# Performance work log

Measured on AMD Instinct MI355X. Metric: run time of the kernel, lower is better.

The kernel has to match this reference:

```python
import jax, jax.numpy as jnp
import numpy as np

B, D, H = 128, 256, 512  # batch, input_size, hidden_size; 2 hidden layers
ORDER = 'A'
EPS = 1e-12


def _masks():
    # Standard MADE sequential degrees: inputs 1..D (reversed for order 'B'),
    # hidden degrees cycle over 1..D-1. Hidden mask: >=, output mask: > (strict).
    din = np.arange(1, D + 1) if ORDER == 'A' else np.arange(D, 0, -1)
    dh = (np.arange(H) % (D - 1)) + 1
    m0 = (dh[:, None] >= din[None, :]).astype(np.float32)  # [H, D]
    m1 = (dh[:, None] >= dh[None, :]).astype(np.float32)   # [H, H]
    mo = (din[:, None] > dh[None, :]).astype(np.float32)   # [D, H]
    return jnp.asarray(m0), jnp.asarray(m1), jnp.asarray(mo)


def _made(y, W0, b0, W1, b1, Wo, bo, masks):
    m0, m1, mo = masks
    h = jax.nn.elu(y @ (W0 * m0).T + b0)   # [B, H]
    h = jax.nn.elu(h @ (W1 * m1).T + b1)   # [B, H]
    return h @ (Wo * mo).T + bo            # [B, D]


def setup_inputs() -> dict:
    key = jax.random.key(0)
    ks = jax.random.split(key, 13)
    s_in, s_h = 1.0 / np.sqrt(D), 1.0 / np.sqrt(H)

    def p(k, shape, s):
        return (jax.random.normal(k, shape, jnp.float32) * s).astype(jnp.float32)

    return {
        'x': jax.random.normal(ks[0], (B, D), jnp.float32),
        'mu_W0': p(ks[1], (H, D), s_in), 'mu_b0': jnp.zeros((H,), jnp.float32),
        'mu_W1': p(ks[2], (H, H), s_h),  'mu_b1': jnp.zeros((H,), jnp.float32),
        'mu_Wo': p(ks[3], (D, H), s_h),  'mu_bo': jnp.zeros((D,), jnp.float32),
        'lv_W0': p(ks[4], (H, D), s_in), 'lv_b0': jnp.zeros((H,), jnp.float32),
        'lv_W1': p(ks[5], (H, H), s_h),  'lv_b1': jnp.zeros((H,), jnp.float32),
        'lv_Wo': p(ks[6], (D, H), s_h),  'lv_bo': jnp.zeros((D,), jnp.float32),
    }


def reference(x, mu_W0, mu_b0, mu_W1, mu_b1, mu_Wo, mu_bo,
              lv_W0, lv_b0, lv_W1, lv_b1, lv_Wo, lv_bo):
    masks = _masks()
    idx = jnp.arange(D) if ORDER == 'A' else jnp.arange(D - 1, -1, -1)

    def step(carry, i):
        y, _ = carry
        mu = _made(y, mu_W0, mu_b0, mu_W1, mu_b1, mu_Wo, mu_bo, masks)
        logstd = 0.5 * _made(y, lv_W0, lv_b0, lv_W1, lv_b1, lv_Wo, lv_bo, masks)
        new_col = (x[:, i] - mu[:, i]) / (jnp.exp(logstd[:, i]) + EPS)
        y = y.at[:, i].set(new_col)
        return (y, logstd), None

    init = (jnp.zeros_like(x), jnp.zeros_like(x))
    (y, logstd), _ = jax.lax.scan(step, init, idx)
    return y, logstd.sum(axis=1)
```

## Files before the change

kernel.cpp:

```cpp
#include <hip/hip_runtime.h>

#define DD 256
#define HH 512
#define BB 128
#define TS 4096

#define WAITVM(N) asm volatile("s_waitcnt vmcnt(" #N ")" ::: "memory")
#define SYNC() do { __builtin_amdgcn_s_barrier(); __builtin_amdgcn_sched_barrier(0); } while (0)

__device__ __forceinline__ float elu_f(float x) {
    return x > 0.f ? x : (__expf(x) - 1.f);
}
__device__ __forceinline__ float rlf(float v, int l) {
    return __uint_as_float(__builtin_amdgcn_readlane(__float_as_uint(v), (unsigned)l));
}
__device__ __forceinline__ float f4c(const float4& v, int r) {
    return r == 0 ? v.x : r == 1 ? v.y : r == 2 ? v.z : v.w;
}

__device__ __forceinline__ int pmap(int h) {
    if (h == 510) return 255;
    if (h == 511) return 511;
    return (h < 255) ? (4 * (h & 63) + (h >> 6))
                     : (256 + 4 * ((h - 255) & 63) + ((h - 255) >> 6));
}
__device__ __forceinline__ int p4map(int j) {
    return 4 * (j & 63) + (j >> 6);
}
__device__ __forceinline__ int w1base(int hp) {
    return (hp <= 254) ? hp * TS
         : (hp <= 509) ? (hp - 255) * TS + 1024
         : 255 * TS + ((hp == 510) ? 0 : 1024);
}
__device__ __forceinline__ int wobase(int hp) {
    return (hp <= 254) ? hp * TS + 3072
         : (hp <= 509) ? (hp - 255) * TS + 3584
         : 255 * TS + ((hp == 510) ? 2048 : 2560);
}

__global__ __launch_bounds__(256) void prep(
    const float* __restrict__ w0m_, const float* __restrict__ w0l_,
    const float* __restrict__ w1m_, const float* __restrict__ w1l_,
    const float* __restrict__ wom_, const float* __restrict__ wol_,
    float* __restrict__ tape)
{
    __shared__ float tm[32][33], tl[32][33];
    const int tx = threadIdx.x & 31, ty = threadIdx.x >> 5;
    const unsigned b = blockIdx.x;

    if (b < 256) {
        const int h0 = (int)(b >> 4) << 5, hp0 = (int)(b & 15) << 5;
        #pragma unroll
        for (int j = 0; j < 4; ++j) {
            int r = ty + 8 * j;
            tm[r][tx] = w1m_[(h0 + r) * HH + hp0 + tx];
            tl[r][tx] = w1l_[(h0 + r) * HH + hp0 + tx];
        }
        __syncthreads();
        #pragma unroll
        for (int j = 0; j < 4; ++j) {
            int hp = hp0 + ty + 8 * j;
            int h  = h0 + tx;
            int dh_h = (h <= 254) ? h + 1 : (h <= 509 ? h - 254 : h - 509);
            int dh_p = (hp <= 254) ? hp + 1 : (hp <= 509 ? hp - 254 : hp - 509);
            float mask = (dh_h >= dh_p) ? 1.f : 0.f;
            int base = w1base(hp), p = pmap(h);
            tape[base + p]       = mask * tm[tx][ty + 8 * j];
            tape[base + 512 + p] = mask * tl[tx][ty + 8 * j];
        }
    } else if (b < 384) {
        const int b2 = (int)b - 256;
        const int h0 = (b2 >> 3) << 5, i0 = (b2 & 7) << 5;
        #pragma unroll
        for (int j = 0; j < 4; ++j) {
            int r = ty + 8 * j;
            tm[r][tx] = w0m_[(h0 + r) * DD + i0 + tx];
            tl[r][tx] = w0l_[(h0 + r) * DD + i0 + tx];
        }
        __syncthreads();
        #pragma unroll
        for (int j = 0; j < 4; ++j) {
            int i = i0 + ty + 8 * j;
            int h = h0 + tx;
            int p = pmap(h);
            tape[i * TS + 2048 + p] = tm[tx][ty + 8 * j];
            tape[i * TS + 2560 + p] = tl[tx][ty + 8 * j];
        }
    } else {
        const int b3 = (int)b - 384;
        const int j0 = (b3 >> 4) << 5, hp0 = (b3 & 15) << 5;
        #pragma unroll
        for (int j = 0; j < 4; ++j) {
            int r = ty + 8 * j;
            tm[r][tx] = wom_[(j0 + r) * HH + hp0 + tx];
            tl[r][tx] = wol_[(j0 + r) * HH + hp0 + tx];
        }
        __syncthreads();
        #pragma unroll
        for (int j = 0; j < 4; ++j) {
            int hp = hp0 + ty + 8 * j;
            int jj = j0 + tx;
            int base = wobase(hp), p = p4map(jj);
            tape[base + p]       = tm[tx][ty + 8 * j];
            tape[base + 256 + p] = tl[tx][ty + 8 * j];
        }
    }
}

struct WSet { float4 w[16]; };

__device__ __forceinline__ void stage16(const float* g, float* l, int lane) {
    #pragma unroll
    for (int k = 0; k < 16; ++k) {
        __builtin_amdgcn_global_load_lds(
            (const __attribute__((address_space(1))) void*)(g + 256 * k + 4 * lane),
            (__attribute__((address_space(3))) void*)(l + 256 * k),
            16, 0, 0);
    }
}

__device__ __forceinline__ void rd_set(WSet& S, const float* b, int lane) {
    const float4* p = (const float4*)b;
    #pragma unroll
    for (int k = 0; k < 16; ++k) S.w[k] = p[64 * k + lane];
}

template<int Q, int EX>
__device__ __forceinline__ void stepC(
    int t, int lane, const WSet& S,
    float (&a0m)[8], float (&a0l)[8], float (&a1m)[8], float (&a1l)[8],
    float (&Rm)[4], float (&Rl)[4], float (&yv)[4],
    const float (&xv)[4], const float (&bmv)[4], const float (&blv)[4],
    float& ls_sum,
    const float4& exmA, const float4& exmB, const float4& exlA, const float4& exlB,
    const float4& exwm, const float4& exwl)
{
    float mu = rlf(Rm[Q], t) + rlf(bmv[Q], t);
    float ls = 0.5f * (rlf(Rl[Q], t) + rlf(blv[Q], t));
    ls_sum += ls;
    float v = __fdividef(rlf(xv[Q], t) - mu, __expf(ls) + 1e-12f);
    yv[Q] = (lane == t) ? v : yv[Q];

    #pragma unroll
    for (int r = Q; r < 4; ++r) {
        a0m[r]     += v * f4c(S.w[8], r);
        a0m[4 + r] += v * f4c(S.w[9], r);
        a0l[r]     += v * f4c(S.w[10], r);
        a0l[4 + r] += v * f4c(S.w[11], r);
    }

    float p0m = elu_f(rlf(a0m[Q], t)),     p0l = elu_f(rlf(a0l[Q], t));
    float p1m = elu_f(rlf(a0m[4 + Q], t)), p1l = elu_f(rlf(a0l[4 + Q], t));
    float p2m = 0.f, p2l = 0.f;
    if (EX) {
        p2m = elu_f(rlf(a0m[EX == 1 ? 3 : 7], 63));
        p2l = elu_f(rlf(a0l[EX == 1 ? 3 : 7], 63));
    }

    #pragma unroll
    for (int r = Q; r < 4; ++r) {
        a1m[r]     += f4c(S.w[0], r) * p0m + f4c(S.w[4], r) * p1m;
        a1m[4 + r] += f4c(S.w[1], r) * p0m + f4c(S.w[5], r) * p1m;
        a1l[r]     += f4c(S.w[2], r) * p0l + f4c(S.w[6], r) * p1l;
        a1l[4 + r] += f4c(S.w[3], r) * p0l + f4c(S.w[7], r) * p1l;
    }
    if (EX) {
        #pragma unroll
        for (int r = 0; r < 4; ++r) {
            a1m[r]     += f4c(exmA, r) * p2m;
            a1m[4 + r] += f4c(exmB, r) * p2m;
            a1l[r]     += f4c(exlA, r) * p2l;
            a1l[4 + r] += f4c(exlB, r) * p2l;
        }
    }

    float q0m = elu_f(rlf(a1m[Q], t)),     q0l = elu_f(rlf(a1l[Q], t));
    float q1m = elu_f(rlf(a1m[4 + Q], t)), q1l = elu_f(rlf(a1l[4 + Q], t));
    float q2m = 0.f, q2l = 0.f;
    if (EX) {
        q2m = elu_f(rlf(a1m[EX == 1 ? 3 : 7], 63));
        q2l = elu_f(rlf(a1l[EX == 1 ? 3 : 7], 63));
    }

    #pragma unroll
    for (int r = Q; r < 4; ++r) {
        Rm[r] += f4c(S.w[12], r) * q0m + f4c(S.w[14], r) * q1m;
        Rl[r] += f4c(S.w[13], r) * q0l + f4c(S.w[15], r) * q1l;
    }
    if (EX) {
        #pragma unroll
        for (int r = 0; r < 4; ++r) {
            Rm[r] += f4c(exwm, r) * q2m;
            Rl[r] += f4c(exwl, r) * q2l;
        }
    }
}

__global__ __launch_bounds__(128, 1) void made_main(
    const float* __restrict__ x,
    const float* __restrict__ mu_b0, const float* __restrict__ mu_b1,
    const float* __restrict__ mu_bo,
    const float* __restrict__ lv_b0, const float* __restrict__ lv_b1,
    const float* __restrict__ lv_bo,
    const float* __restrict__ tape,
    float* __restrict__ out)
{
    __shared__ __align__(16) float buf[4][TS];
    const int row = blockIdx.x;

    if (threadIdx.x >= 64) {
        const int lane = threadIdx.x - 64;
        #pragma unroll
        for (int g = 0; g < 3; ++g)
            stage16(tape + (size_t)g * TS, &buf[g][0], lane);
        #pragma unroll 1
        for (int t = 0; t < 255; ++t) {
            if (t < 253) { WAITVM(16); } else { WAITVM(0); }
            __builtin_amdgcn_s_barrier();
            __builtin_amdgcn_sched_barrier(0);
            int g = t + 3;
            if (g < 255)
                stage16(tape + (size_t)g * TS, &buf[g & 3][0], lane);
        }
        return;
    }

    const int lane = threadIdx.x;

    float a0m[8], a0l[8], a1m[8], a1l[8], Rm[4], Rl[4], yv[4];
    float xv[4], bmv[4], blv[4];
    #pragma unroll
    for (int r = 0; r < 4; ++r) {
        a0m[r]     = mu_b0[lane + 64 * r];
        a0m[4 + r] = mu_b0[255 + lane + 64 * r];
        a0l[r]     = lv_b0[lane + 64 * r];
        a0l[4 + r] = lv_b0[255 + lane + 64 * r];
        a1m[r]     = mu_b1[lane + 64 * r];
        a1m[4 + r] = mu_b1[255 + lane + 64 * r];
        a1l[r]     = lv_b1[lane + 64 * r];
        a1l[4 + r] = lv_b1[255 + lane + 64 * r];
        Rm[r] = 0.f; Rl[r] = 0.f; yv[r] = 0.f;
        xv[r]  = x[row * DD + 64 * r + lane];
        bmv[r] = mu_bo[64 * r + lane];
        blv[r] = lv_bo[64 * r + lane];
    }
    if (lane == 63) {
        a0m[3] = mu_b0[510]; a0m[7] = mu_b0[511];
        a0l[3] = lv_b0[510]; a0l[7] = lv_b0[511];
        a1m[3] = mu_b1[510]; a1m[7] = mu_b1[511];
        a1l[3] = lv_b1[510]; a1l[7] = lv_b1[511];
    }

    const float4* a4 = (const float4*)(tape + 255 * TS);
    float4 e510mA = a4[lane],       e510mB = a4[64 + lane];
    float4 e510lA = a4[128 + lane], e510lB = a4[192 + lane];
    float4 e511mA = a4[256 + lane], e511mB = a4[320 + lane];
    float4 e511lA = a4[384 + lane], e511lB = a4[448 + lane];
    float4 wo510m = a4[512 + lane], wo510l = a4[576 + lane];
    float4 wo511m = a4[640 + lane], wo511l = a4[704 + lane];

    const float4 d4 = make_float4(0.f, 0.f, 0.f, 0.f);

    float ls_sum = 0.f;
    WSet A, B;

    SYNC();
    rd_set(A, &buf[0][0], lane);
    rd_set(B, &buf[1][0], lane);
    stepC<0, 1>(0, lane, A, a0m, a0l, a1m, a1l, Rm, Rl, yv, xv, bmv, blv,
                ls_sum, e510mA, e510mB, e510lA, e510lB, wo510m, wo510l);

    SYNC();
    rd_set(A, &buf[2][0], lane);
    stepC<0, 2>(1, lane, B, a0m, a0l, a1m, a1l, Rm, Rl, yv, xv, bmv, blv,
                ls_sum, e511mA, e511mB, e511lA, e511lB, wo511m, wo511l);

#define PAIR_BODY(Q, t, tl)                                                   \
    {                                                                         \
        SYNC();                                                               \
        rd_set(B, &buf[((t) + 1) & 3][0], lane);                              \
        stepC<Q, 0>((tl), lane, A, a0m, a0l, a1m, a1l, Rm, Rl, yv,            \
                    xv, bmv, blv, ls_sum, d4, d4, d4, d4, d4, d4);            \
        SYNC();                                                               \
        rd_set(A, &buf[((t) + 2) & 3][0], lane);                              \
        stepC<Q, 0>((tl) + 1, lane, B, a0m, a0l, a1m, a1l, Rm, Rl, yv,        \
                    xv, bmv, blv, ls_sum, d4, d4, d4, d4, d4, d4);            \
    }

    #pragma unroll 1
    for (int t = 2; t < 64; t += 2)    PAIR_BODY(0, t, t)
    #pragma unroll 1
    for (int t = 64; t < 128; t += 2)  PAIR_BODY(1, t, t - 64)
    #pragma unroll 1
    for (int t = 128; t < 192; t += 2) PAIR_BODY(2, t, t - 128)
    #pragma unroll 1
    for (int t = 192; t < 254; t += 2) PAIR_BODY(3, t, t - 192)
#undef PAIR_BODY

    SYNC();
    stepC<3, 0>(62, lane, A, a0m, a0l, a1m, a1l, Rm, Rl, yv, xv, bmv, blv,
                ls_sum, d4, d4, d4, d4, d4, d4);

    {
        float mu = rlf(Rm[3], 63) + rlf(bmv[3], 63);
        float ls = 0.5f * (rlf(Rl[3], 63) + rlf(blv[3], 63));
        ls_sum += ls;
        float v = __fdividef(rlf(xv[3], 63) - mu, __expf(ls) + 1e-12f);
        yv[3] = (lane == 63) ? v : yv[3];
    }

    #pragma unroll
    for (int r = 0; r < 4; ++r) out[row * DD + 64 * r + lane] = yv[r];
    if (lane == 0) out[BB * DD + row] = ls_sum;
}

extern "C" void kernel_launch(void* const* d_in, const int* in_sizes, int n_in,
                              void* d_out, int out_size, void* d_ws, size_t ws_size,
                              hipStream_t stream) {
    const float* x     = (const float*)d_in[0];
    const float* mu_W0 = (const float*)d_in[1];
    const float* mu_b0 = (const float*)d_in[2];
    const float* mu_W1 = (const float*)d_in[3];
    const float* mu_b1 = (const float*)d_in[4];
    const float* mu_Wo = (const float*)d_in[5];
    const float* mu_bo = (const float*)d_in[6];
    const float* lv_W0 = (const float*)d_in[7];
    const float* lv_b0 = (const float*)d_in[8];
    const float* lv_W1 = (const float*)d_in[9];
    const float* lv_b1 = (const float*)d_in[10];
    const float* lv_Wo = (const float*)d_in[11];
    const float* lv_bo = (const float*)d_in[12];

    float* tape = (float*)d_ws;

    prep<<<512, 256, 0, stream>>>(mu_W0, lv_W0, mu_W1, lv_W1, mu_Wo, lv_Wo, tape);
    made_main<<<BB, 128, 0, stream>>>(x, mu_b0, mu_b1, mu_bo,
                                      lv_b0, lv_b1, lv_bo, tape, (float*)d_out);
}
```

Measured before the change: 183.1 us.

## Stage tape in pairs to halve producer-consumer barriers per step

The producer wave now loads two tape slices per barrier into a double-buffered pair of slots. The consumer reads both slices and runs two steps between barriers instead of one. This halves the number of workgroup barriers in the serial 255-step loop. In exchange, prefetch depth drops from three slices in flight to a wait-all per pair, so load latency is less hidden, and register pressure rises because two weight sets are live at once.

Measured after the change: 185.9 us. No clear change (+1.5%).

```diff
diff --git a/kernel.cpp b/kernel.cpp
--- a/kernel.cpp
+++ b/kernel.cpp
@@ -210,17 +210,17 @@
 
     if (threadIdx.x >= 64) {
         const int lane = threadIdx.x - 64;
-        #pragma unroll
-        for (int g = 0; g < 3; ++g)
-            stage16(tape + (size_t)g * TS, &buf[g][0], lane);
+        stage16(tape + 0 * TS, &buf[0][0], lane);
+        stage16(tape + 1 * TS, &buf[1][0], lane);
         #pragma unroll 1
-        for (int t = 0; t < 255; ++t) {
-            if (t < 253) { WAITVM(16); } else { WAITVM(0); }
+        for (int T = 0; T < 128; ++T) {
+            WAITVM(0);
             __builtin_amdgcn_s_barrier();
             __builtin_amdgcn_sched_barrier(0);
-            int g = t + 3;
-            if (g < 255)
-                stage16(tape + (size_t)g * TS, &buf[g & 3][0], lane);
+            int g0 = 2 * (T + 1), g1 = g0 + 1;
+            int f  = (T + 1) & 1;
+            if (g0 < 255) stage16(tape + (size_t)g0 * TS, &buf[2 * f][0], lane);
+            if (g1 < 255) stage16(tape + (size_t)g1 * TS, &buf[2 * f + 1][0], lane);
         }
         return;
     }
@@ -269,35 +269,33 @@
     rd_set(B, &buf[1][0], lane);
     stepC<0, 1>(0, lane, A, a0m, a0l, a1m, a1l, Rm, Rl, yv, xv, bmv, blv,
                 ls_sum, e510mA, e510mB, e510lA, e510lB, wo510m, wo510l);
+    stepC<0, 2>(1, lane, B, a0m, a0l, a1m, a1l, Rm, Rl, yv, xv, bmv, blv,
+                ls_sum, e511mA, e511mB, e511lA, e511lB, wo511m, wo511l);
+
+#define PAIR_BODY(Q, T)                                                       \
+    {                                                                         \
+        SYNC();                                                               \
+        const int f_ = (T) & 1;                                               \
+        rd_set(A, &buf[2 * f_][0], lane);                                     \
+        rd_set(B, &buf[2 * f_ + 1][0], lane);                                 \
+        stepC<Q, 0>(2 * (T) - 64 * (Q), lane, A, a0m, a0l, a1m, a1l,          \
+                    Rm, Rl, yv, xv, bmv, blv, ls_sum, d4, d4, d4, d4, d4, d4);\
+        stepC<Q, 0>(2 * (T) + 1 - 64 * (Q), lane, B, a0m, a0l, a1m, a1l,     \
+                    Rm, Rl, yv, xv, bmv, blv, ls_sum, d4, d4, d4, d4, d4, d4);\
+    }
+
+    #pragma unroll 1
+    for (int T = 1; T < 32; ++T)   PAIR_BODY(0, T)
+    #pragma unroll 1
+    for (int T = 32; T < 64; ++T)  PAIR_BODY(1, T)
+    #pragma unroll 1
+    for (int T = 64; T < 96; ++T)  PAIR_BODY(2, T)
+    #pragma unroll 1
+    for (int T = 96; T < 127; ++T) PAIR_BODY(3, T)
+#undef PAIR_BODY
 
     SYNC();
     rd_set(A, &buf[2][0], lane);
-    stepC<0, 2>(1, lane, B, a0m, a0l, a1m, a1l, Rm, Rl, yv, xv, bmv, blv,
-                ls_sum, e511mA, e511mB, e511lA, e511lB, wo511m, wo511l);
-
-#define PAIR_BODY(Q, t, tl)                                                   \
-    {                                                                         \
-        SYNC();                                                               \
-        rd_set(B, &buf[((t) + 1) & 3][0], lane);                              \
-        stepC<Q, 0>((tl), lane, A, a0m, a0l, a1m, a1l, Rm, Rl, yv,            \
-                    xv, bmv, blv, ls_sum, d4, d4, d4, d4, d4, d4);            \
-        SYNC();                                                               \
-        rd_set(A, &buf[((t) + 2) & 3][0], lane);                              \
-        stepC<Q, 0>((tl) + 1, lane, B, a0m, a0l, a1m, a1l, Rm, Rl, yv,        \
-                    xv, bmv, blv, ls_sum, d4, d4, d4, d4, d4, d4);            \
-    }
-
-    #pragma unroll 1
-    for (int t = 2; t < 64; t += 2)    PAIR_BODY(0, t, t)
-    #pragma unroll 1
-    for (int t = 64; t < 128; t += 2)  PAIR_BODY(1, t, t - 64)
-    #pragma unroll 1
-    for (int t = 128; t < 192; t += 2) PAIR_BODY(2, t, t - 128)
-    #pragma unroll 1
-    for (int t = 192; t < 254; t += 2) PAIR_BODY(3, t, t - 192)
-#undef PAIR_BODY
-
-    SYNC();
     stepC<3, 0>(62, lane, A, a0m, a0l, a1m, a1l, Rm, Rl, yv, xv, bmv, blv,
                 ls_sum, d4, d4, d4, d4, d4, d4);
 
```
